# Optimization experiments

Measured on AMD Instinct MI355X. Metric: run time of the kernel, lower is better.

## Reference

```python
import jax, jax.numpy as jnp
import numpy as np

L_OUT, B, N, C, M, D, T = 4, 4, 1000, 80, 64, 256, 28
CLS_W, L1_W, GIOU_W, MASK_W = 2.0, 5.0, 2.0, 5.0
ALPHA, GAMMA, EPS = 0.25, 2.0, 1e-8
CANDIDATE_K, CENTER_RADIUS, BIG = 10, 2.5, 100000.0


def _areas(b):
    return (b[..., 2] - b[..., 0]) * (b[..., 3] - b[..., 1])


def pairwise_giou(b1, b2):
    # b1 [n,4], b2 [m,4] -> [n,m] generalized IoU (torchvision convention)
    area1, area2 = _areas(b1), _areas(b2)
    lt = jnp.maximum(b1[:, None, :2], b2[None, :, :2])
    rb = jnp.minimum(b1[:, None, 2:], b2[None, :, 2:])
    wh = jnp.clip(rb - lt, 0.0)
    inter = wh[..., 0] * wh[..., 1]
    union = area1[:, None] + area2[None, :] - inter
    iou = inter / union
    lti = jnp.minimum(b1[:, None, :2], b2[None, :, :2])
    rbi = jnp.maximum(b1[:, None, 2:], b2[None, :, 2:])
    whi = jnp.clip(rbi - lti, 0.0)
    areai = whi[..., 0] * whi[..., 1]
    return iou - (areai - union) / areai


def diag_giou(b1, b2):
    # elementwise giou for matched pairs, b1/b2 [n,4] -> [n]
    area1, area2 = _areas(b1), _areas(b2)
    lt = jnp.maximum(b1[:, :2], b2[:, :2])
    rb = jnp.minimum(b1[:, 2:], b2[:, 2:])
    wh = jnp.clip(rb - lt, 0.0)
    inter = wh[:, 0] * wh[:, 1]
    union = area1 + area2 - inter
    iou = inter / union
    lti = jnp.minimum(b1[:, :2], b2[:, :2])
    rbi = jnp.maximum(b1[:, 2:], b2[:, 2:])
    whi = jnp.clip(rbi - lti, 0.0)
    areai = whi[:, 0] * whi[:, 1]
    return iou - (areai - union) / areai


def pairwise_iou(b1, b2, eps=1e-8):
    # mmdet bbox_overlaps, mode='iou'
    area1, area2 = _areas(b1), _areas(b2)
    lt = jnp.maximum(b1[:, None, :2], b2[None, :, :2])
    rb = jnp.minimum(b1[:, None, 2:], b2[None, :, 2:])
    wh = jnp.clip(rb - lt, 0.0)
    inter = wh[..., 0] * wh[..., 1]
    union = jnp.maximum(area1[:, None] + area2[None, :] - inter, eps)
    return inter / union


def simota_match(logits, boxes, gt_cls, gt_boxes, img_size):
    # SimOTA assignment for one image; fixed shapes via masking instead of boolean indexing
    n, c = logits.shape
    m = gt_boxes.shape[0]
    cx = (boxes[:, 0] + boxes[:, 2]) * 0.5
    cy = (boxes[:, 1] + boxes[:, 3]) * 0.5
    w = boxes[:, 2] - boxes[:, 0]
    h = boxes[:, 3] - boxes[:, 1]
    in_gt = ((cx[:, None] > gt_boxes[None, :, 0]) & (cy[:, None] > gt_boxes[None, :, 1])
             & (cx[:, None] < gt_boxes[None, :, 2]) & (cy[:, None] < gt_boxes[None, :, 3]))
    gcx = (gt_boxes[:, 0] + gt_boxes[:, 2]) * 0.5
    gcy = (gt_boxes[:, 1] + gt_boxes[:, 3]) * 0.5
    rx = CENTER_RADIUS * w[:, None]
    ry = CENTER_RADIUS * h[:, None]
    in_ct = ((cx[:, None] > gcx[None, :] - rx) & (cx[:, None] < gcx[None, :] + rx)
             & (cy[:, None] > gcy[None, :] - ry) & (cy[:, None] < gcy[None, :] + ry))
    valid = in_gt.any(1) | in_ct.any(1)
    in_both = in_gt & in_ct
    has_valid = valid.any()
    valid = valid | (~has_valid)          # fallback: all valid when none
    in_both = in_both | (~has_valid)
    # FocalLossCost (mmdet), weight = cls weight
    p = jax.nn.sigmoid(logits)
    neg = -jnp.log(1.0 - p + EPS) * (1.0 - ALPHA) * p ** GAMMA
    pos = -jnp.log(p + EPS) * ALPHA * (1.0 - p) ** GAMMA
    cls_cost = CLS_W * (pos - neg)[:, gt_cls]          # [n,m]
    nb = boxes / img_size
    ngb = gt_boxes / img_size
    l1_cost = L1_W * jnp.abs(nb[:, None, :] - ngb[None, :, :]).sum(-1)
    giou_cost = GIOU_W * (1.0 - pairwise_giou(nb, ngb))
    cost = cls_cost + l1_cost + giou_cost + (~in_both) * BIG
    cost = jnp.where(valid[:, None], cost, 1e15)       # invalid priors never selected
    ious = pairwise_iou(boxes, gt_boxes) * valid[:, None]
    # dynamic_k_matching
    topk_ious, _ = jax.lax.top_k(ious.T, CANDIDATE_K)  # [m,10]
    dyn_k = jnp.maximum(topk_ious.sum(-1).astype(jnp.int32), 1)
    rank = jnp.argsort(jnp.argsort(cost, axis=0), axis=0)
    matching = rank < dyn_k[None, :]                   # [n,m]
    multi = matching.sum(1) > 1
    best = jnp.argmin(cost, axis=1)
    best_oh = best[:, None] == jnp.arange(m)[None, :]
    matching = jnp.where(multi[:, None], best_oh, matching)
    fg = matching.any(1)
    gt_ind = jnp.argmax(matching, axis=1)
    return fg, gt_ind


def per_image_loss(logits, boxes, pfeat, gt_cls, gt_boxes, gt_masks, img_size, w_mask):
    sg = jax.lax.stop_gradient
    fg, gt_ind = simota_match(sg(logits), sg(boxes), gt_cls, sg(gt_boxes), sg(img_size))
    c = logits.shape[1]
    gcls = gt_cls[gt_ind]
    label = jnp.where(fg[:, None], jax.nn.one_hot(gcls, c, dtype=logits.dtype), 0.0)
    # sigmoid focal loss (sum over all n*c logits)
    p = jax.nn.sigmoid(logits)
    ce = -(label * jax.nn.log_sigmoid(logits) + (1.0 - label) * jax.nn.log_sigmoid(-logits))
    p_t = p * label + (1.0 - p) * (1.0 - label)
    alpha_t = ALPHA * label + (1.0 - ALPHA) * (1.0 - label)
    cls_loss = (alpha_t * ce * (1.0 - p_t) ** GAMMA).sum()
    fgf = fg.astype(logits.dtype)
    nb = boxes / img_size
    gb = gt_boxes[gt_ind] / img_size
    l1_loss = (jnp.abs(nb - gb).sum(-1) * fgf).sum()
    giou_loss = ((1.0 - diag_giou(nb, gb)) * fgf).sum()
    # mask head: per-class mask logits from proposal feats; gather only assigned class
    d = pfeat.shape[1]
    tt = T * T
    w_sel = w_mask.reshape(d, c, tt)[:, gcls, :]        # [d,n,tt]
    m_sel = jax.nn.sigmoid(jnp.einsum('nd,dnt->nt', pfeat, w_sel))
    gm = gt_masks.reshape(gt_masks.shape[0], -1)[gt_ind]  # [n,tt]
    inter = (m_sel * gm).sum(-1)
    union = m_sel.sum(-1) + gm.sum(-1) + 1e-8
    mask_loss = ((1.0 - 2.0 * inter / union) * fgf).sum()
    return cls_loss, l1_loss, giou_loss, mask_loss, fgf.sum()


def _forward(pred_logits, pred_boxes, proposal_feat, gt_boxes, gt_masks, image_size, w_mask, gt_classes):
    per = jax.vmap(per_image_loss, in_axes=(0, 0, 0, 0, 0, 0, 0, None))
    total = jnp.zeros(4, dtype=pred_logits.dtype)
    n_out = pred_logits.shape[0]
    for l in range(n_out):   # small fixed loop over output heads
        cl, l1, gl, ml, k = per(pred_logits[l], pred_boxes[l], proposal_feat[l],
                                gt_classes, gt_boxes, gt_masks, image_size, w_mask)
        num_ins = k.sum()
        total = total + jnp.stack([cl.sum(), l1.sum(), gl.sum(), ml.sum()]) / num_ins
    weights = jnp.array([CLS_W, L1_W, GIOU_W, MASK_W], dtype=total.dtype)
    return weights * total / n_out   # [cls, l1, giou, mask] losses


def setup_inputs():
    key = jax.random.key(0)
    ks = jax.random.split(key, 8)

    def rand_boxes(k, shape):
        k1, k2 = jax.random.split(k)
        ctr = jax.random.uniform(k1, shape + (2,), minval=100.0, maxval=700.0)
        wh = jax.random.uniform(k2, shape + (2,), minval=20.0, maxval=300.0)
        return jnp.concatenate([ctr - wh * 0.5, ctr + wh * 0.5], axis=-1)

    pred_logits = jax.random.normal(ks[0], (L_OUT, B, N, C), dtype=jnp.float32)
    pred_boxes = rand_boxes(ks[1], (L_OUT, B, N))
    proposal_feat = 0.1 * jax.random.normal(ks[2], (L_OUT, B, N, D), dtype=jnp.float32)
    gt_boxes = rand_boxes(ks[3], (B, M))
    gt_masks = (jax.random.uniform(ks[4], (B, M, T, T)) > 0.5).astype(jnp.float32)
    image_size = 800.0 * jnp.ones((B,), dtype=jnp.float32)
    w_mask = 0.02 * jax.random.normal(ks[5], (D, C * T * T), dtype=jnp.float32)
    gt_classes = jax.random.randint(ks[6], (B, M), 0, C)
    return {"pred_logits": pred_logits, "pred_boxes": pred_boxes, "proposal_feat": proposal_feat,
            "gt_boxes": gt_boxes, "gt_masks": gt_masks, "image_size": image_size,
            "w_mask": w_mask, "gt_classes": gt_classes}


def reference(pred_logits, pred_boxes, proposal_feat, gt_boxes, gt_masks, image_size, w_mask, gt_classes):
    return _forward(pred_logits, pred_boxes, proposal_feat, gt_boxes, gt_masks, image_size, w_mask, gt_classes)
```

## Files before the change

kernel.cpp:

```cpp
#include <hip/hip_runtime.h>
#include <math.h>
#include <float.h>

#define LOUT 4
#define BATCH 4
#define NP 1000
#define NC 80
#define NM 64
#define ND 256
#define TT 784
#define NIMG (LOUT*BATCH)
#define CWTT (NC*TT)
#define MAXF (NIMG*NP)
#define CH 32
#define TPT 112
#define MAXCH 408

__device__ __forceinline__ float block_reduce_sum(float v, float* red) {
    int tid = threadIdx.x;
    red[tid] = v; __syncthreads();
    for (int s = blockDim.x >> 1; s > 0; s >>= 1) {
        if (tid < s) red[tid] += red[tid + s];
        __syncthreads();
    }
    float r = red[0]; __syncthreads();
    return r;
}

__global__ void k_valid(const float* __restrict__ boxes, const float* __restrict__ gtb,
                        int* __restrict__ valid, unsigned long long* __restrict__ inboth,
                        int* __restrict__ hasvalid) {
    int img = blockIdx.y;
    int b = img % BATCH;
    int i = blockIdx.x * blockDim.x + threadIdx.x;
    __shared__ float g[NM * 4];
    for (int k = threadIdx.x; k < NM * 4; k += blockDim.x) g[k] = gtb[b * NM * 4 + k];
    __syncthreads();
    if (i >= NP) return;
    float4 bx = *(const float4*)&boxes[((size_t)img * NP + i) * 4];
    float x0 = bx.x, y0 = bx.y, x1 = bx.z, y1 = bx.w;
    float cx = (x0 + x1) * 0.5f, cy = (y0 + y1) * 0.5f;
    float w = x1 - x0, h = y1 - y0;
    float rx = 2.5f * w, ry = 2.5f * h;
    bool any_gt = false, any_ct = false;
    unsigned long long ib = 0ull;
    for (int j = 0; j < NM; ++j) {
        float gx0 = g[j*4], gy0 = g[j*4+1], gx1 = g[j*4+2], gy1 = g[j*4+3];
        bool igt = (cx > gx0) && (cy > gy0) && (cx < gx1) && (cy < gy1);
        float gcx = (gx0 + gx1) * 0.5f, gcy = (gy0 + gy1) * 0.5f;
        bool ict = (cx > gcx - rx) && (cx < gcx + rx) && (cy > gcy - ry) && (cy < gcy + ry);
        any_gt |= igt; any_ct |= ict;
        if (igt && ict) ib |= (1ull << j);
    }
    bool v = any_gt || any_ct;
    valid[img * NP + i] = v ? 1 : 0;
    inboth[img * NP + i] = ib;
    if (v) atomicOr(&hasvalid[img], 1);
}

__global__ void __launch_bounds__(256) k_costtopk(
        const float* __restrict__ logits, const float* __restrict__ boxes,
        const float* __restrict__ gtb, const int* __restrict__ gcls_all,
        const float* __restrict__ imsz,
        const int* __restrict__ valid, const unsigned long long* __restrict__ inboth,
        const int* __restrict__ hasvalid,
        float* __restrict__ cost, float* __restrict__ kthc, int* __restrict__ kthi) {
    int j = blockIdx.x, img = blockIdx.y, b = img % BATCH;
    float s = imsz[b], inv_s = 1.f / s;
    const float* gj = gtb + (b * NM + j) * 4;
    float gx0 = gj[0], gy0 = gj[1], gx1 = gj[2], gy1 = gj[3];
    int gc = gcls_all[b * NM + j];
    int hv = hasvalid[img];
    float garea = (gx1 - gx0) * (gy1 - gy0);
    float ngx0 = gx0 * inv_s, ngy0 = gy0 * inv_s, ngx1 = gx1 * inv_s, ngy1 = gy1 * inv_s;
    float ngarea = (ngx1 - ngx0) * (ngy1 - ngy0);
    size_t colbase = ((size_t)img * NM + j) * NP;
    int tid = threadIdx.x;
    float icv[4], ccv[4];
    #pragma unroll
    for (int e = 0; e < 4; ++e) {
        int i = tid + 256 * e;
        if (i < NP) {
            float4 bx = *(const float4*)&boxes[((size_t)img * NP + i) * 4];
            float x0 = bx.x, y0 = bx.y, x1 = bx.z, y1 = bx.w;
            float area = (x1 - x0) * (y1 - y0);
            float ltx = fmaxf(x0, gx0), lty = fmaxf(y0, gy0);
            float rbx = fminf(x1, gx1), rby = fminf(y1, gy1);
            float iw = fmaxf(rbx - ltx, 0.f), ih = fmaxf(rby - lty, 0.f);
            float inter = iw * ih;
            float uni = fmaxf(area + garea - inter, 1e-8f);
            float iou = inter / uni;
            float nx0 = x0 * inv_s, ny0 = y0 * inv_s, nx1 = x1 * inv_s, ny1 = y1 * inv_s;
            float narea = (nx1 - nx0) * (ny1 - ny0);
            float nltx = fmaxf(nx0, ngx0), nlty = fmaxf(ny0, ngy0);
            float nrbx = fminf(nx1, ngx1), nrby = fminf(ny1, ngy1);
            float niw = fmaxf(nrbx - nltx, 0.f), nih = fmaxf(nrby - nlty, 0.f);
            float ninter = niw * nih;
            float nuni = narea + ngarea - ninter;
            float niou = ninter / nuni;
            float ex0 = fminf(nx0, ngx0), ey0 = fminf(ny0, ngy0);
            float ex1 = fmaxf(nx1, ngx1), ey1 = fmaxf(ny1, ngy1);
            float earea = fmaxf(ex1 - ex0, 0.f) * fmaxf(ey1 - ey0, 0.f);
            float giou = niou - (earea - nuni) / earea;
            float giou_cost = 2.f * (1.f - giou);
            float l1 = 5.f * (fabsf(nx0 - ngx0) + fabsf(ny0 - ngy0) + fabsf(nx1 - ngx1) + fabsf(ny1 - ngy1));
            float x = logits[((size_t)img * NP + i) * NC + gc];
            float p = 1.f / (1.f + expf(-x));
            float neg = -logf(1.f - p + 1e-8f) * 0.75f * p * p;
            float pos = -logf(p + 1e-8f) * 0.25f * (1.f - p) * (1.f - p);
            float cls = 2.f * (pos - neg);
            bool vld = (valid[img * NP + i] != 0) || (hv == 0);
            bool inb = (((inboth[img * NP + i] >> j) & 1ull) != 0ull) || (hv == 0);
            float cst = cls + l1 + giou_cost + (inb ? 0.f : 100000.f);
            if (!vld) cst = 1e15f;
            cost[colbase + i] = cst;
            ccv[e] = cst;
            icv[e] = vld ? iou : 0.f;
        } else {
            ccv[e] = FLT_MAX;
            icv[e] = -FLT_MAX;
        }
    }
    __shared__ float wv[4]; __shared__ int wi[4];
    int wave = tid >> 6, lane = tid & 63;
    unsigned cons = 0;
    float ssum = 0.f;
    for (int it = 0; it < 10; ++it) {
        float bv = -FLT_MAX; int bi = NP;
        #pragma unroll
        for (int e = 0; e < 4; ++e) {
            int i = tid + 256 * e;
            float v = icv[e];
            if (!(cons & (1u << e)) && ((v > bv) || (v == bv && i < bi))) { bv = v; bi = i; }
        }
        #pragma unroll
        for (int sft = 1; sft < 64; sft <<= 1) {
            float ov = __shfl_xor(bv, sft, 64);
            int oi = __shfl_xor(bi, sft, 64);
            if ((ov > bv) || (ov == bv && oi < bi)) { bv = ov; bi = oi; }
        }
        if (lane == 0) { wv[wave] = bv; wi[wave] = bi; }
        __syncthreads();
        float gv = wv[0]; int gi = wi[0];
        #pragma unroll
        for (int w = 1; w < 4; ++w) {
            float ov = wv[w]; int oi = wi[w];
            if ((ov > gv) || (ov == gv && oi < gi)) { gv = ov; gi = oi; }
        }
        __syncthreads();
        ssum += gv;
        if ((gi & 255) == tid) cons |= (1u << (gi >> 8));
    }
    int dk = (int)ssum; if (dk < 1) dk = 1;
    cons = 0;
    float gvf = 0.f; int gif = 0;
    for (int it = 0; it < dk; ++it) {
        float bv = FLT_MAX; int bi = NP;
        #pragma unroll
        for (int e = 0; e < 4; ++e) {
            int i = tid + 256 * e;
            float v = ccv[e];
            if (!(cons & (1u << e)) && ((v < bv) || (v == bv && i < bi))) { bv = v; bi = i; }
        }
        #pragma unroll
        for (int sft = 1; sft < 64; sft <<= 1) {
            float ov = __shfl_xor(bv, sft, 64);
            int oi = __shfl_xor(bi, sft, 64);
            if ((ov < bv) || (ov == bv && oi < bi)) { bv = ov; bi = oi; }
        }
        if (lane == 0) { wv[wave] = bv; wi[wave] = bi; }
        __syncthreads();
        float gv = wv[0]; int gi = wi[0];
        #pragma unroll
        for (int w = 1; w < 4; ++w) {
            float ov = wv[w]; int oi = wi[w];
            if ((ov < gv) || (ov == gv && oi < gi)) { gv = ov; gi = oi; }
        }
        __syncthreads();
        if ((gi & 255) == tid) cons |= (1u << (gi >> 8));
        gvf = gv; gif = gi;
    }
    if (tid == 0) { kthc[blockIdx.y * NM + j] = gvf; kthi[blockIdx.y * NM + j] = gif; }
}

__global__ void k_match(const float* __restrict__ cost,
                        const float* __restrict__ kthc, const int* __restrict__ kthi,
                        const float* __restrict__ boxes, const float* __restrict__ gtb,
                        const float* __restrict__ imsz, const int* __restrict__ gcls_all,
                        int* __restrict__ fg, int* __restrict__ gt_ind,
                        int* __restrict__ cnt, float* __restrict__ accum) {
    int img = blockIdx.y, b = img % BATCH;
    int i = blockIdx.x * blockDim.x + threadIdx.x;
    __shared__ float skc[NM]; __shared__ int ski[NM];
    __shared__ float red[256];
    if (threadIdx.x < NM) {
        skc[threadIdx.x] = kthc[img * NM + threadIdx.x];
        ski[threadIdx.x] = kthi[img * NM + threadIdx.x];
    }
    __syncthreads();
    float l1 = 0.f, gl = 0.f, f = 0.f;
    if (i < NP) {
        int cntm = 0, first = -1;
        float bc = FLT_MAX; int bj = 0;
        for (int j = 0; j < NM; ++j) {
            float c = cost[((size_t)img * NM + j) * NP + i];
            bool m = (c < skc[j]) || (c == skc[j] && i <= ski[j]);
            if (m) { cntm++; if (first < 0) first = j; }
            if (c < bc) { bc = c; bj = j; }
        }
        int gi = 0, isfg = 0;
        if (cntm > 1) { gi = bj; isfg = 1; }
        else if (cntm == 1) { gi = first; isfg = 1; }
        fg[img * NP + i] = isfg;
        gt_ind[img * NP + i] = gi;
        if (isfg) {
            atomicAdd(&cnt[gcls_all[b * NM + gi]], 1);
            float inv = 1.f / imsz[b];
            float4 bx = *(const float4*)&boxes[((size_t)img * NP + i) * 4];
            const float* gj = gtb + (b * NM + gi) * 4;
            float nx0 = bx.x*inv, ny0 = bx.y*inv, nx1 = bx.z*inv, ny1 = bx.w*inv;
            float gx0 = gj[0]*inv, gy0 = gj[1]*inv, gx1 = gj[2]*inv, gy1 = gj[3]*inv;
            l1 = fabsf(nx0-gx0) + fabsf(ny0-gy0) + fabsf(nx1-gx1) + fabsf(ny1-gy1);
            float a1 = (nx1-nx0)*(ny1-ny0), a2 = (gx1-gx0)*(gy1-gy0);
            float ltx = fmaxf(nx0,gx0), lty = fmaxf(ny0,gy0);
            float rbx = fminf(nx1,gx1), rby = fminf(ny1,gy1);
            float iw = fmaxf(rbx-ltx,0.f), ih = fmaxf(rby-lty,0.f);
            float inter = iw*ih, uni = a1+a2-inter, iou = inter/uni;
            float ex0 = fminf(nx0,gx0), ey0 = fminf(ny0,gy0);
            float ex1 = fmaxf(nx1,gx1), ey1 = fmaxf(ny1,gy1);
            float ea = fmaxf(ex1-ex0,0.f)*fmaxf(ey1-ey0,0.f);
            float giou = iou - (ea-uni)/ea;
            gl = 1.f - giou;
            f = 1.f;
        }
    }
    float sl1 = block_reduce_sum(l1, red);
    float sgl = block_reduce_sum(gl, red);
    float sf  = block_reduce_sum(f, red);
    if (threadIdx.x == 0) {
        atomicAdd(&accum[img*5+1], sl1);
        atomicAdd(&accum[img*5+2], sgl);
        atomicAdd(&accum[img*5+4], sf);
    }
}

__global__ void k_focal(const float* __restrict__ logits, const int* __restrict__ fg,
                        const int* __restrict__ gt_ind, const int* __restrict__ gcls_all,
                        float* __restrict__ accum) {
    int img = blockIdx.y, b = img % BATCH;
    int idx = blockIdx.x * blockDim.x + threadIdx.x;
    __shared__ float red[256];
    float v = 0.f;
    if (idx < NP * NC) {
        int i = idx / NC, c = idx % NC;
        float x = logits[(size_t)img * NP * NC + idx];
        int lab = 0;
        if (fg[img * NP + i]) {
            int gc = gcls_all[b * NM + gt_ind[img * NP + i]];
            lab = (c == gc) ? 1 : 0;
        }
        float p = 1.f / (1.f + expf(-x));
        float ax = fabsf(x);
        float sp = log1pf(expf(-ax));
        float ls_pos = fminf(x, 0.f) - sp;
        float ls_neg = fminf(-x, 0.f) - sp;
        if (lab) v = 0.25f * (-ls_pos) * (1.f - p) * (1.f - p);
        else     v = 0.75f * (-ls_neg) * p * p;
    }
    float sv = block_reduce_sum(v, red);
    if (threadIdx.x == 0) atomicAdd(&accum[img*5+0], sv);
}

__global__ void k_gmsum(const float* __restrict__ gtm, float* __restrict__ gmsum) {
    int bj = blockIdx.x;
    __shared__ float red[128];
    float s = 0.f;
    for (int t = threadIdx.x; t < TT; t += 128) s += gtm[(size_t)bj * TT + t];
    int tid = threadIdx.x;
    red[tid] = s; __syncthreads();
    for (int st = 64; st > 0; st >>= 1) {
        if (tid < st) red[tid] += red[tid + st];
        __syncthreads();
    }
    if (tid == 0) gmsum[bj] = red[0];
}

__global__ void __launch_bounds__(1024) k_scanscatter(
        const int* __restrict__ cnt, const int* __restrict__ fg,
        const int* __restrict__ gti, const int* __restrict__ gcls,
        int* __restrict__ offs_g, int* __restrict__ total,
        int* __restrict__ chtab, int* __restrict__ nch, int* __restrict__ list) {
    __shared__ int offs[NC]; __shared__ int choff[NC]; __shared__ int sfill[NC];
    int tid = threadIdx.x;
    if (tid == 0) {
        int s = 0, m = 0;
        for (int c = 0; c < NC; ++c) {
            offs[c] = s; s += cnt[c];
            choff[c] = m; m += (cnt[c] + CH - 1) / CH;
        }
        *total = s; *nch = m;
    }
    if (tid < NC) sfill[tid] = 0;
    __syncthreads();
    if (tid < NC) {
        offs_g[tid] = offs[tid];
        int n = cnt[tid], co = choff[tid];
        for (int k = 0; k * CH < n; ++k) chtab[co + k] = (tid << 16) | k;
    }
    for (int idx = tid; idx < NIMG * NP; idx += 1024) {
        if (fg[idx]) {
            int img = idx / NP, i = idx % NP, b = img % BATCH;
            int gt = gti[idx];
            int c = gcls[b * NM + gt];
            int pos = offs[c] + atomicAdd(&sfill[c], 1);
            list[pos] = (img << 16) | (gt << 10) | i;
        }
    }
}

__global__ void __launch_bounds__(128) k_mgemm(
        const float* __restrict__ pfeat, const float* __restrict__ wmask,
        const float* __restrict__ gtm, const int* __restrict__ list,
        const int* __restrict__ cnt, const int* __restrict__ offs,
        const int* __restrict__ chtab, const int* __restrict__ nch,
        float* __restrict__ inter, float* __restrict__ msum) {
    int ch = blockIdx.x;
    if (ch >= *nch) return;
    int e = chtab[ch];
    int c = e >> 16, k = e & 0xffff;
    int base = offs[c] + k * CH;
    int P = min(CH, cnt[c] - k * CH);
    int tid = threadIdx.x;
    bool act = (tid < TPT);
    int t = blockIdx.y * TPT + (act ? tid : 0);
    __shared__ float pf[CH][ND];
    __shared__ int sl[CH];
    if (tid < CH) sl[tid] = (tid < P) ? list[base + tid] : 0;
    __syncthreads();
    for (int idx = tid; idx < CH * (ND / 4); idx += 128) {
        int p = idx >> 6, d4 = idx & 63;
        float4 v = {0.f, 0.f, 0.f, 0.f};
        if (p < P) {
            int pk = sl[p];
            int img = pk >> 16, i = pk & 1023;
            v = *(const float4*)&pfeat[((size_t)img * NP + i) * ND + d4 * 4];
        }
        *(float4*)&pf[p][d4 * 4] = v;
    }
    __syncthreads();
    float acc[CH];
    #pragma unroll
    for (int p = 0; p < CH; ++p) acc[p] = 0.f;
    if (act) {
        const float* wr = wmask + (size_t)c * TT + t;
        float4 wq[4];
        #pragma unroll
        for (int q = 0; q < 4; ++q) {
            const float* wp = wr + (size_t)q * 4 * CWTT;
            wq[q].x = wp[0]; wq[q].y = wp[CWTT];
            wq[q].z = wp[2 * (size_t)CWTT]; wq[q].w = wp[3 * (size_t)CWTT];
        }
        #pragma unroll 4
        for (int d4 = 0; d4 < 60; ++d4) {
            float4 w = wq[d4 & 3];
            const float* wp = wr + (size_t)(d4 + 4) * 4 * CWTT;
            wq[d4 & 3].x = wp[0]; wq[d4 & 3].y = wp[CWTT];
            wq[d4 & 3].z = wp[2 * (size_t)CWTT]; wq[d4 & 3].w = wp[3 * (size_t)CWTT];
            int d = d4 * 4;
            #pragma unroll
            for (int p = 0; p < CH; ++p) {
                float4 q4 = *(const float4*)&pf[p][d];
                acc[p] += q4.x * w.x + q4.y * w.y + q4.z * w.z + q4.w * w.w;
            }
        }
        #pragma unroll
        for (int d4 = 60; d4 < 64; ++d4) {
            float4 w = wq[d4 & 3];
            int d = d4 * 4;
            #pragma unroll
            for (int p = 0; p < CH; ++p) {
                float4 q4 = *(const float4*)&pf[p][d];
                acc[p] += q4.x * w.x + q4.y * w.y + q4.z * w.z + q4.w * w.w;
            }
        }
    }
    #pragma unroll 4
    for (int p = 0; p < CH; ++p) {
        if (p >= P) break;
        int pk = sl[p];
        int img = pk >> 16, j = (pk >> 10) & 63, b = img % BATCH;
        float li = 0.f, lm = 0.f;
        if (act) {
            float m = 1.f / (1.f + expf(-acc[p]));
            float g = gtm[((size_t)(b * NM + j)) * TT + t];
            li = m * g; lm = m;
        }
        #pragma unroll
        for (int s = 32; s > 0; s >>= 1) {
            li += __shfl_down(li, s, 64);
            lm += __shfl_down(lm, s, 64);
        }
        if ((tid & 63) == 0) {
            atomicAdd(&inter[base + p], li);
            atomicAdd(&msum[base + p], lm);
        }
    }
}

__global__ void __launch_bounds__(256) k_dicefinal(
        const int* __restrict__ list, const int* __restrict__ total,
        const float* __restrict__ inter, const float* __restrict__ msum,
        const float* __restrict__ gmsum, const float* __restrict__ accum,
        float* __restrict__ out) {
    __shared__ float md[NIMG];
    int tid = threadIdx.x;
    if (tid < NIMG) md[tid] = 0.f;
    __syncthreads();
    int n = *total;
    for (int e = tid; e < n; e += 256) {
        int pk = list[e];
        int img = pk >> 16, j = (pk >> 10) & 63, b = img % BATCH;
        float d = 1.f - 2.f * inter[e] / (msum[e] + gmsum[b * NM + j] + 1e-8f);
        atomicAdd(&md[img], d);
    }
    __syncthreads();
    if (tid == 0) {
        float tot[4] = {0.f, 0.f, 0.f, 0.f};
        for (int l = 0; l < LOUT; ++l) {
            float s0 = 0.f, s1 = 0.f, s2 = 0.f, s3 = 0.f, s4 = 0.f;
            for (int b = 0; b < BATCH; ++b) {
                int img = l * BATCH + b;
                s0 += accum[img*5+0]; s1 += accum[img*5+1]; s2 += accum[img*5+2];
                s3 += md[img];        s4 += accum[img*5+4];
            }
            tot[0] += s0 / s4; tot[1] += s1 / s4; tot[2] += s2 / s4; tot[3] += s3 / s4;
        }
        const float w[4] = {2.f, 5.f, 2.f, 5.f};
        for (int k = 0; k < 4; ++k) out[k] = w[k] * tot[k] / (float)LOUT;
    }
}

extern "C" void kernel_launch(void* const* d_in, const int* in_sizes, int n_in,
                              void* d_out, int out_size, void* d_ws, size_t ws_size,
                              hipStream_t stream) {
    const float* logits = (const float*)d_in[0];
    const float* boxes  = (const float*)d_in[1];
    const float* pfeat  = (const float*)d_in[2];
    const float* gtb    = (const float*)d_in[3];
    const float* gtm    = (const float*)d_in[4];
    const float* imsz   = (const float*)d_in[5];
    const float* wmask  = (const float*)d_in[6];
    const int*   gcls   = (const int*)d_in[7];

    char* ws = (char*)d_ws;
    size_t off = 0;
    auto alloc = [&](size_t bytes) -> void* {
        void* p = ws + off;
        off = (off + bytes + 255) & ~(size_t)255;
        return p;
    };
    char* zbase = ws;
    float* accum = (float*)alloc(NIMG * 5 * sizeof(float));
    int* cnt    = (int*)alloc(NC * sizeof(int));
    int* hasvalid = (int*)alloc(NIMG * sizeof(int));
    float* interA = (float*)alloc((size_t)MAXF * sizeof(float));
    float* msumA  = (float*)alloc((size_t)MAXF * sizeof(float));
    size_t zbytes = off;
    float* cost = (float*)alloc((size_t)NIMG * NM * NP * sizeof(float));
    int* valid  = (int*)alloc((size_t)NIMG * NP * sizeof(int));
    unsigned long long* inboth = (unsigned long long*)alloc((size_t)NIMG * NP * sizeof(unsigned long long));
    float* kthc = (float*)alloc(NIMG * NM * sizeof(float));
    int* kthi   = (int*)alloc(NIMG * NM * sizeof(int));
    int* fg     = (int*)alloc((size_t)NIMG * NP * sizeof(int));
    int* gti    = (int*)alloc((size_t)NIMG * NP * sizeof(int));
    float* gmsum = (float*)alloc(BATCH * NM * sizeof(float));
    int* offs   = (int*)alloc(NC * sizeof(int));
    int* total  = (int*)alloc(sizeof(int));
    int* nch    = (int*)alloc(sizeof(int));
    int* chtab  = (int*)alloc((size_t)MAXCH * sizeof(int));
    int* list   = (int*)alloc((size_t)MAXF * sizeof(int));

    hipMemsetAsync(zbase, 0, zbytes, stream);

    k_gmsum<<<BATCH * NM, 128, 0, stream>>>(gtm, gmsum);
    k_valid<<<dim3((NP + 255) / 256, NIMG), 256, 0, stream>>>(boxes, gtb, valid, inboth, hasvalid);
    k_costtopk<<<dim3(NM, NIMG), 256, 0, stream>>>(logits, boxes, gtb, gcls, imsz, valid, inboth, hasvalid, cost, kthc, kthi);
    k_match<<<dim3((NP + 255) / 256, NIMG), 256, 0, stream>>>(cost, kthc, kthi, boxes, gtb, imsz, gcls, fg, gti, cnt, accum);
    k_focal<<<dim3((NP * NC + 255) / 256, NIMG), 256, 0, stream>>>(logits, fg, gti, gcls, accum);
    k_scanscatter<<<1, 1024, 0, stream>>>(cnt, fg, gti, gcls, offs, total, chtab, nch, list);
    k_mgemm<<<dim3(MAXCH, (TT + TPT - 1) / TPT), 128, 0, stream>>>(pfeat, wmask, gtm, list, cnt, offs, chtab, nch, interA, msumA);
    k_dicefinal<<<1, 256, 0, stream>>>(list, total, interA, msumA, gmsum, accum, (float*)d_out);
}
```

Before: 237.4 us.

## Fuse prep kernels, transpose logits, wave-level top-k, fold focal loss into match

Merges gt-mask sums, validity masks, a logits transpose and per-proposal negative focal sums into one multi-role prep kernel. The cost/top-k kernel now handles one GT per wavefront with 16 elements per lane, which removes block-level barriers, and it reads logits from the transposed copy with coalesced loads. The separate dense focal kernel is removed and its positive-class correction moves into the match kernel. Mask GEMM chunk size is halved with more chunk slots. This trades extra transpose traffic and workspace for fewer launches and syncs.

```diff
diff --git a/kernel.cpp b/kernel.cpp
--- a/kernel.cpp
+++ b/kernel.cpp
@@ -12,9 +12,9 @@
 #define NIMG (LOUT*BATCH)
 #define CWTT (NC*TT)
 #define MAXF (NIMG*NP)
-#define CH 32
+#define CH 16
 #define TPT 112
-#define MAXCH 408
+#define MAXCH 768
 
 __device__ __forceinline__ float block_reduce_sum(float v, float* red) {
     int tid = threadIdx.x;
@@ -27,45 +27,98 @@
     return r;
 }
 
-__global__ void k_valid(const float* __restrict__ boxes, const float* __restrict__ gtb,
-                        int* __restrict__ valid, unsigned long long* __restrict__ inboth,
-                        int* __restrict__ hasvalid) {
-    int img = blockIdx.y;
-    int b = img % BATCH;
-    int i = blockIdx.x * blockDim.x + threadIdx.x;
-    __shared__ float g[NM * 4];
-    for (int k = threadIdx.x; k < NM * 4; k += blockDim.x) g[k] = gtb[b * NM * 4 + k];
-    __syncthreads();
-    if (i >= NP) return;
-    float4 bx = *(const float4*)&boxes[((size_t)img * NP + i) * 4];
-    float x0 = bx.x, y0 = bx.y, x1 = bx.z, y1 = bx.w;
-    float cx = (x0 + x1) * 0.5f, cy = (y0 + y1) * 0.5f;
-    float w = x1 - x0, h = y1 - y0;
-    float rx = 2.5f * w, ry = 2.5f * h;
-    bool any_gt = false, any_ct = false;
-    unsigned long long ib = 0ull;
-    for (int j = 0; j < NM; ++j) {
-        float gx0 = g[j*4], gy0 = g[j*4+1], gx1 = g[j*4+2], gy1 = g[j*4+3];
-        bool igt = (cx > gx0) && (cy > gy0) && (cx < gx1) && (cy < gy1);
-        float gcx = (gx0 + gx1) * 0.5f, gcy = (gy0 + gy1) * 0.5f;
-        bool ict = (cx > gcx - rx) && (cx < gcx + rx) && (cy > gcy - ry) && (cy < gcy + ry);
-        any_gt |= igt; any_ct |= ict;
-        if (igt && ict) ib |= (1ull << j);
-    }
-    bool v = any_gt || any_ct;
-    valid[img * NP + i] = v ? 1 : 0;
-    inboth[img * NP + i] = ib;
-    if (v) atomicOr(&hasvalid[img], 1);
+__global__ void __launch_bounds__(256) k_prep(
+        const float* __restrict__ logits, const float* __restrict__ boxes,
+        const float* __restrict__ gtb, const float* __restrict__ gtm,
+        int* __restrict__ valid, unsigned long long* __restrict__ inboth,
+        int* __restrict__ hasvalid, float* __restrict__ logT,
+        float* __restrict__ negsum, float* __restrict__ gmsum) {
+    int blk = blockIdx.x;
+    int tid = threadIdx.x;
+    __shared__ float red[256];
+    __shared__ float tile[32][33];
+    if (blk < 256) {
+        int bj = blk;
+        float s = 0.f;
+        for (int t = tid; t < TT; t += 256) s += gtm[(size_t)bj * TT + t];
+        float r = block_reduce_sum(s, red);
+        if (tid == 0) gmsum[bj] = r;
+    } else if (blk < 320) {
+        int rel = blk - 256;
+        int img = rel >> 2, q = rel & 3, b = img % BATCH;
+        float* g = red;
+        g[tid] = gtb[b * NM * 4 + tid];
+        __syncthreads();
+        int i = q * 256 + tid;
+        if (i >= NP) return;
+        float4 bx = *(const float4*)&boxes[((size_t)img * NP + i) * 4];
+        float x0 = bx.x, y0 = bx.y, x1 = bx.z, y1 = bx.w;
+        float cx = (x0 + x1) * 0.5f, cy = (y0 + y1) * 0.5f;
+        float w = x1 - x0, h = y1 - y0;
+        float rx = 2.5f * w, ry = 2.5f * h;
+        bool any_gt = false, any_ct = false;
+        unsigned long long ib = 0ull;
+        for (int j = 0; j < NM; ++j) {
+            float gx0 = g[j*4], gy0 = g[j*4+1], gx1 = g[j*4+2], gy1 = g[j*4+3];
+            bool igt = (cx > gx0) && (cy > gy0) && (cx < gx1) && (cy < gy1);
+            float gcx = (gx0 + gx1) * 0.5f, gcy = (gy0 + gy1) * 0.5f;
+            bool ict = (cx > gcx - rx) && (cx < gcx + rx) && (cy > gcy - ry) && (cy < gcy + ry);
+            any_gt |= igt; any_ct |= ict;
+            if (igt && ict) ib |= (1ull << j);
+        }
+        bool v = any_gt || any_ct;
+        valid[img * NP + i] = v ? 1 : 0;
+        inboth[img * NP + i] = ib;
+        if (v) atomicOr(&hasvalid[img], 1);
+    } else if (blk < 1856) {
+        int rel = blk - 320;
+        int img = rel / 96; int r2 = rel % 96;
+        int i0 = (r2 / 3) * 32, c0 = (r2 % 3) * 32;
+        int tx = tid & 31, ty4 = tid >> 5;
+        #pragma unroll
+        for (int r = 0; r < 4; ++r) {
+            int ty = ty4 + r * 8;
+            int i = i0 + ty, c = c0 + tx;
+            tile[ty][tx] = (i < NP && c < NC) ? logits[((size_t)img * NP + i) * NC + c] : 0.f;
+        }
+        __syncthreads();
+        #pragma unroll
+        for (int r = 0; r < 4; ++r) {
+            int ty = ty4 + r * 8;
+            int c = c0 + ty, i = i0 + tx;
+            if (c < NC && i < NP) logT[((size_t)img * NC + c) * NP + i] = tile[tx][ty];
+        }
+    } else {
+        int rel = blk - 1856;
+        int img = rel >> 2, q = rel & 3;
+        int i = q * 256 + tid;
+        if (i >= NP) return;
+        const float* lr = logits + ((size_t)img * NP + i) * NC;
+        float s = 0.f;
+        #pragma unroll 4
+        for (int c = 0; c < NC; ++c) {
+            float x = lr[c];
+            float p = 1.f / (1.f + expf(-x));
+            float ax = fabsf(x);
+            float sp = log1pf(expf(-ax));
+            float ls_neg = fminf(-x, 0.f) - sp;
+            s += 0.75f * (-ls_neg) * p * p;
+        }
+        negsum[img * NP + i] = s;
+    }
 }
 
 __global__ void __launch_bounds__(256) k_costtopk(
-        const float* __restrict__ logits, const float* __restrict__ boxes,
+        const float* __restrict__ logT, const float* __restrict__ boxes,
         const float* __restrict__ gtb, const int* __restrict__ gcls_all,
         const float* __restrict__ imsz,
         const int* __restrict__ valid, const unsigned long long* __restrict__ inboth,
         const int* __restrict__ hasvalid,
         float* __restrict__ cost, float* __restrict__ kthc, int* __restrict__ kthi) {
-    int j = blockIdx.x, img = blockIdx.y, b = img % BATCH;
+    int img = blockIdx.y, b = img % BATCH;
+    int tid = threadIdx.x;
+    int w = tid >> 6, l = tid & 63;
+    int j = blockIdx.x * 4 + w;
     float s = imsz[b], inv_s = 1.f / s;
     const float* gj = gtb + (b * NM + j) * 4;
     float gx0 = gj[0], gy0 = gj[1], gx1 = gj[2], gy1 = gj[3];
@@ -75,11 +128,11 @@
     float ngx0 = gx0 * inv_s, ngy0 = gy0 * inv_s, ngx1 = gx1 * inv_s, ngy1 = gy1 * inv_s;
     float ngarea = (ngx1 - ngx0) * (ngy1 - ngy0);
     size_t colbase = ((size_t)img * NM + j) * NP;
-    int tid = threadIdx.x;
-    float icv[4], ccv[4];
+    const float* lrow = logT + ((size_t)img * NC + gc) * NP;
+    float icv[16], ccv[16];
     #pragma unroll
-    for (int e = 0; e < 4; ++e) {
-        int i = tid + 256 * e;
+    for (int e = 0; e < 16; ++e) {
+        int i = e * 64 + l;
         if (i < NP) {
             float4 bx = *(const float4*)&boxes[((size_t)img * NP + i) * 4];
             float x0 = bx.x, y0 = bx.y, x1 = bx.z, y1 = bx.w;
@@ -104,7 +157,7 @@
             float giou = niou - (earea - nuni) / earea;
             float giou_cost = 2.f * (1.f - giou);
             float l1 = 5.f * (fabsf(nx0 - ngx0) + fabsf(ny0 - ngy0) + fabsf(nx1 - ngx1) + fabsf(ny1 - ngy1));
-            float x = logits[((size_t)img * NP + i) * NC + gc];
+            float x = lrow[i];
             float p = 1.f / (1.f + expf(-x));
             float neg = -logf(1.f - p + 1e-8f) * 0.75f * p * p;
             float pos = -logf(p + 1e-8f) * 0.25f * (1.f - p) * (1.f - p);
@@ -121,17 +174,15 @@
             icv[e] = -FLT_MAX;
         }
     }
-    __shared__ float wv[4]; __shared__ int wi[4];
-    int wave = tid >> 6, lane = tid & 63;
     unsigned cons = 0;
     float ssum = 0.f;
     for (int it = 0; it < 10; ++it) {
-        float bv = -FLT_MAX; int bi = NP;
-        #pragma unroll
-        for (int e = 0; e < 4; ++e) {
-            int i = tid + 256 * e;
-            float v = icv[e];
-            if (!(cons & (1u << e)) && ((v > bv) || (v == bv && i < bi))) { bv = v; bi = i; }
+        float bv = -FLT_MAX; int bi = 0x7fffffff;
+        #pragma unroll
+        for (int e = 0; e < 16; ++e) {
+            if (cons & (1u << e)) continue;
+            float v = icv[e]; int i = e * 64 + l;
+            if ((v > bv) || (v == bv && i < bi)) { bv = v; bi = i; }
         }
         #pragma unroll
         for (int sft = 1; sft < 64; sft <<= 1) {
@@ -139,28 +190,19 @@
             int oi = __shfl_xor(bi, sft, 64);
             if ((ov > bv) || (ov == bv && oi < bi)) { bv = ov; bi = oi; }
         }
-        if (lane == 0) { wv[wave] = bv; wi[wave] = bi; }
-        __syncthreads();
-        float gv = wv[0]; int gi = wi[0];
-        #pragma unroll
-        for (int w = 1; w < 4; ++w) {
-            float ov = wv[w]; int oi = wi[w];
-            if ((ov > gv) || (ov == gv && oi < gi)) { gv = ov; gi = oi; }
-        }
-        __syncthreads();
-        ssum += gv;
-        if ((gi & 255) == tid) cons |= (1u << (gi >> 8));
+        ssum += bv;
+        if ((bi & 63) == l) cons |= 1u << (bi >> 6);
     }
     int dk = (int)ssum; if (dk < 1) dk = 1;
     cons = 0;
-    float gvf = 0.f; int gif = 0;
+    float gv = 0.f; int gi = 0;
     for (int it = 0; it < dk; ++it) {
-        float bv = FLT_MAX; int bi = NP;
-        #pragma unroll
-        for (int e = 0; e < 4; ++e) {
-            int i = tid + 256 * e;
-            float v = ccv[e];
-            if (!(cons & (1u << e)) && ((v < bv) || (v == bv && i < bi))) { bv = v; bi = i; }
+        float bv = FLT_MAX; int bi = 0x7fffffff;
+        #pragma unroll
+        for (int e = 0; e < 16; ++e) {
+            if (cons & (1u << e)) continue;
+            float v = ccv[e]; int i = e * 64 + l;
+            if ((v < bv) || (v == bv && i < bi)) { bv = v; bi = i; }
         }
         #pragma unroll
         for (int sft = 1; sft < 64; sft <<= 1) {
@@ -168,25 +210,17 @@
             int oi = __shfl_xor(bi, sft, 64);
             if ((ov < bv) || (ov == bv && oi < bi)) { bv = ov; bi = oi; }
         }
-        if (lane == 0) { wv[wave] = bv; wi[wave] = bi; }
-        __syncthreads();
-        float gv = wv[0]; int gi = wi[0];
-        #pragma unroll
-        for (int w = 1; w < 4; ++w) {
-            float ov = wv[w]; int oi = wi[w];
-            if ((ov < gv) || (ov == gv && oi < gi)) { gv = ov; gi = oi; }
-        }
-        __syncthreads();
-        if ((gi & 255) == tid) cons |= (1u << (gi >> 8));
-        gvf = gv; gif = gi;
-    }
-    if (tid == 0) { kthc[blockIdx.y * NM + j] = gvf; kthi[blockIdx.y * NM + j] = gif; }
+        if ((bi & 63) == l) cons |= 1u << (bi >> 6);
+        gv = bv; gi = bi;
+    }
+    if (l == 0) { kthc[img * NM + j] = gv; kthi[img * NM + j] = gi; }
 }
 
 __global__ void k_match(const float* __restrict__ cost,
                         const float* __restrict__ kthc, const int* __restrict__ kthi,
                         const float* __restrict__ boxes, const float* __restrict__ gtb,
                         const float* __restrict__ imsz, const int* __restrict__ gcls_all,
+                        const float* __restrict__ negsum, const float* __restrict__ logT,
                         int* __restrict__ fg, int* __restrict__ gt_ind,
                         int* __restrict__ cnt, float* __restrict__ accum) {
     int img = blockIdx.y, b = img % BATCH;
@@ -198,8 +232,9 @@
         ski[threadIdx.x] = kthi[img * NM + threadIdx.x];
     }
     __syncthreads();
-    float l1 = 0.f, gl = 0.f, f = 0.f;
+    float l1 = 0.f, gl = 0.f, f = 0.f, vcls = 0.f;
     if (i < NP) {
+        vcls = negsum[img * NP + i];
         int cntm = 0, first = -1;
         float bc = FLT_MAX; int bj = 0;
         for (int j = 0; j < NM; ++j) {
@@ -214,7 +249,17 @@
         fg[img * NP + i] = isfg;
         gt_ind[img * NP + i] = gi;
         if (isfg) {
-            atomicAdd(&cnt[gcls_all[b * NM + gi]], 1);
+            int gc = gcls_all[b * NM + gi];
+            atomicAdd(&cnt[gc], 1);
+            float x = logT[((size_t)img * NC + gc) * NP + i];
+            float p = 1.f / (1.f + expf(-x));
+            float ax = fabsf(x);
+            float sp = log1pf(expf(-ax));
+            float ls_pos = fminf(x, 0.f) - sp;
+            float ls_neg = fminf(-x, 0.f) - sp;
+            float pos = 0.25f * (-ls_pos) * (1.f - p) * (1.f - p);
+            float neg = 0.75f * (-ls_neg) * p * p;
+            vcls += pos - neg;
             float inv = 1.f / imsz[b];
             float4 bx = *(const float4*)&boxes[((size_t)img * NP + i) * 4];
             const float* gj = gtb + (b * NM + gi) * 4;
@@ -234,55 +279,16 @@
             f = 1.f;
         }
     }
+    float scl = block_reduce_sum(vcls, red);
     float sl1 = block_reduce_sum(l1, red);
     float sgl = block_reduce_sum(gl, red);
     float sf  = block_reduce_sum(f, red);
     if (threadIdx.x == 0) {
+        atomicAdd(&accum[img*5+0], scl);
         atomicAdd(&accum[img*5+1], sl1);
         atomicAdd(&accum[img*5+2], sgl);
         atomicAdd(&accum[img*5+4], sf);
     }
-}
-
-__global__ void k_focal(const float* __restrict__ logits, const int* __restrict__ fg,
-                        const int* __restrict__ gt_ind, const int* __restrict__ gcls_all,
-                        float* __restrict__ accum) {
-    int img = blockIdx.y, b = img % BATCH;
-    int idx = blockIdx.x * blockDim.x + threadIdx.x;
-    __shared__ float red[256];
-    float v = 0.f;
-    if (idx < NP * NC) {
-        int i = idx / NC, c = idx % NC;
-        float x = logits[(size_t)img * NP * NC + idx];
-        int lab = 0;
-        if (fg[img * NP + i]) {
-            int gc = gcls_all[b * NM + gt_ind[img * NP + i]];
-            lab = (c == gc) ? 1 : 0;
-        }
-        float p = 1.f / (1.f + expf(-x));
-        float ax = fabsf(x);
-        float sp = log1pf(expf(-ax));
-        float ls_pos = fminf(x, 0.f) - sp;
-        float ls_neg = fminf(-x, 0.f) - sp;
-        if (lab) v = 0.25f * (-ls_pos) * (1.f - p) * (1.f - p);
-        else     v = 0.75f * (-ls_neg) * p * p;
-    }
-    float sv = block_reduce_sum(v, red);
-    if (threadIdx.x == 0) atomicAdd(&accum[img*5+0], sv);
-}
-
-__global__ void k_gmsum(const float* __restrict__ gtm, float* __restrict__ gmsum) {
-    int bj = blockIdx.x;
-    __shared__ float red[128];
-    float s = 0.f;
-    for (int t = threadIdx.x; t < TT; t += 128) s += gtm[(size_t)bj * TT + t];
-    int tid = threadIdx.x;
-    red[tid] = s; __syncthreads();
-    for (int st = 64; st > 0; st >>= 1) {
-        if (tid < st) red[tid] += red[tid + st];
-        __syncthreads();
-    }
-    if (tid == 0) gmsum[bj] = red[0];
 }
 
 __global__ void __launch_bounds__(1024) k_scanscatter(
@@ -467,6 +473,8 @@
     float* msumA  = (float*)alloc((size_t)MAXF * sizeof(float));
     size_t zbytes = off;
     float* cost = (float*)alloc((size_t)NIMG * NM * NP * sizeof(float));
+    float* logT = (float*)alloc((size_t)NIMG * NC * NP * sizeof(float));
+    float* negsum = (float*)alloc((size_t)NIMG * NP * sizeof(float));
     int* valid  = (int*)alloc((size_t)NIMG * NP * sizeof(int));
     unsigned long long* inboth = (unsigned long long*)alloc((size_t)NIMG * NP * sizeof(unsigned long long));
     float* kthc = (float*)alloc(NIMG * NM * sizeof(float));
@@ -482,12 +490,10 @@
 
     hipMemsetAsync(zbase, 0, zbytes, stream);
 
-    k_gmsum<<<BATCH * NM, 128, 0, stream>>>(gtm, gmsum);
-    k_valid<<<dim3((NP + 255) / 256, NIMG), 256, 0, stream>>>(boxes, gtb, valid, inboth, hasvalid);
-    k_costtopk<<<dim3(NM, NIMG), 256, 0, stream>>>(logits, boxes, gtb, gcls, imsz, valid, inboth, hasvalid, cost, kthc, kthi);
-    k_match<<<dim3((NP + 255) / 256, NIMG), 256, 0, stream>>>(cost, kthc, kthi, boxes, gtb, imsz, gcls, fg, gti, cnt, accum);
-    k_focal<<<dim3((NP * NC + 255) / 256, NIMG), 256, 0, stream>>>(logits, fg, gti, gcls, accum);
+    k_prep<<<1920, 256, 0, stream>>>(logits, boxes, gtb, gtm, valid, inboth, hasvalid, logT, negsum, gmsum);
+    k_costtopk<<<dim3(NM / 4, NIMG), 256, 0, stream>>>(logT, boxes, gtb, gcls, imsz, valid, inboth, hasvalid, cost, kthc, kthi);
+    k_match<<<dim3((NP + 255) / 256, NIMG), 256, 0, stream>>>(cost, kthc, kthi, boxes, gtb, imsz, gcls, negsum, logT, fg, gti, cnt, accum);
     k_scanscatter<<<1, 1024, 0, stream>>>(cnt, fg, gti, gcls, offs, total, chtab, nch, list);
-    k_mgemm<<<dim3(MAXCH, (TT + TPT - 1) / TPT), 128, 0, stream>>>(pfeat, wmask, gtm, list, cnt, offs, chtab, nch, interA, msumA);
+    k_mgemm<<<dim3(MAXCH, 7), 128, 0, stream>>>(pfeat, wmask, gtm, list, cnt, offs, chtab, nch, interA, msumA);
     k_dicefinal<<<1, 256, 0, stream>>>(list, total, interA, msumA, gmsum, accum, (float*)d_out);
 }
```

Result: faster. 200.7 us (-15.4%).
